# Kernel tuning notes

Measured on AMD Instinct MI355X. Metric: run time of the kernel, lower is better.

## Reference

```python
import jax, jax.numpy as jnp
import numpy as np

D = 1024; H = 16; DKV = 64; DFF = 4096
NB = 32; MAXD = 128
B = 4; LD = 1024; LE = 1024
NEG = -1e9
EPS = 1e-6


def setup_inputs():
    key = jax.random.key(0)
    ks = jax.random.split(key, 13)
    s = 0.02
    def W(k, shape):
        return jax.random.normal(k, shape, jnp.float32) * s
    return {
        "encoder_hidden_states": jax.random.normal(ks[0], (B, LE, D), jnp.float32),
        "hidden_states": jax.random.normal(ks[1], (B, LD, D), jnp.float32),
        "ln1_w": jnp.ones((D,), jnp.float32),
        "sa_q": W(ks[2], (D, H * DKV)),
        "sa_k": W(ks[3], (D, H * DKV)),
        "sa_v": W(ks[4], (D, H * DKV)),
        "sa_o": W(ks[5], (H * DKV, D)),
        "rel_bias": W(ks[6], (NB, H)),
        "ln2_w": jnp.ones((D,), jnp.float32),
        "ca_q": W(ks[7], (D, H * DKV)),
        "ca_k": W(ks[8], (D, H * DKV)),
        "ca_v": W(ks[9], (D, H * DKV)),
        "ca_o": W(ks[10], (H * DKV, D)),
        "ln3_w": jnp.ones((D,), jnp.float32),
        "wi": W(ks[11], (D, DFF)),
        "wo": W(ks[12], (DFF, D)),
        "final_ln_w": jnp.ones((D,), jnp.float32),
        "encoder_attention_mask": jnp.ones((B, LE), jnp.int32),
        "attention_mask": jnp.ones((B, LD), jnp.int32),
    }


def _rms(x, w):
    # T5 LayerNorm: RMS norm, no mean subtraction, no bias
    var = jnp.mean(x * x, axis=-1, keepdims=True)
    return x * jax.lax.rsqrt(var + EPS) * w


def _rel_bucket(rp):
    # T5 relative position bucketing, non-bidirectional (decoder causal)
    n = -jnp.minimum(rp, 0)
    max_exact = NB // 2
    is_small = n < max_exact
    nf = jnp.maximum(n, 1).astype(jnp.float32)
    val_large = max_exact + (
        jnp.log(nf / max_exact) / np.log(MAXD / max_exact) * (NB - max_exact)
    ).astype(jnp.int32)
    val_large = jnp.minimum(val_large, NB - 1)
    return jnp.where(is_small, n, val_large)


def _attn(xq, xkv, Wq, Wk, Wv, Wo, bias):
    b, lq, _ = xq.shape
    lk = xkv.shape[1]
    q = (xq @ Wq).reshape(b, lq, H, DKV)
    k = (xkv @ Wk).reshape(b, lk, H, DKV)
    v = (xkv @ Wv).reshape(b, lk, H, DKV)
    # T5: no 1/sqrt(d) scaling; additive position bias + mask before softmax
    scores = jnp.einsum('bqhd,bkhd->bhqk', q, k) + bias
    p = jax.nn.softmax(scores, axis=-1)
    o = jnp.einsum('bhqk,bkhd->bqhd', p, v).reshape(b, lq, H * DKV)
    return o @ Wo


def reference(encoder_hidden_states, hidden_states, ln1_w, sa_q, sa_k, sa_v, sa_o,
              rel_bias, ln2_w, ca_q, ca_k, ca_v, ca_o, ln3_w, wi, wo, final_ln_w,
              encoder_attention_mask, attention_mask):
    b, ld, _ = hidden_states.shape
    q_pos = jnp.arange(ld)[:, None]
    k_pos = jnp.arange(ld)[None, :]
    pos_bias = rel_bias[_rel_bucket(k_pos - q_pos)].transpose(2, 0, 1)[None]  # [1,H,LD,LD]
    # decoder extended mask: causal AND padding
    self_ok = (k_pos <= q_pos)[None, None] & (attention_mask[:, None, None, :] > 0)
    self_bias = pos_bias + jnp.where(self_ok, 0.0, NEG)
    # cross-attention: encoder padding mask; enc-dec position bias is zeros
    cross_bias = jnp.where(encoder_attention_mask[:, None, None, :] > 0, 0.0, NEG)

    h = hidden_states
    x = _rms(h, ln1_w)
    h = h + _attn(x, x, sa_q, sa_k, sa_v, sa_o, self_bias)
    x = _rms(h, ln2_w)
    h = h + _attn(x, encoder_hidden_states, ca_q, ca_k, ca_v, ca_o, cross_bias)
    x = _rms(h, ln3_w)
    h = h + jax.nn.relu(x @ wi) @ wo
    return _rms(h, final_ln_w)
```

## Files before the change

### kernel.cpp

```cpp
#include <hip/hip_runtime.h>


#define BB   4
#define LDEC 1024
#define LENC 1024
#define DIM  1024
#define NH   16
#define DK   64
#define DFFN 4096
#define NEGF (-1e9f)

typedef unsigned short u16;
typedef __attribute__((ext_vector_type(8))) unsigned short u16x8;
typedef __attribute__((ext_vector_type(8))) short s16x8;
typedef __attribute__((ext_vector_type(4))) float f32x4;

__device__ __forceinline__ float bf2f(u16 u) {
    union { unsigned int i; float f; } c; c.i = ((unsigned int)u) << 16; return c.f;
}
__device__ __forceinline__ u16 f2bf(float f) {
    union { float f; unsigned int i; } c; c.f = f;
    unsigned int x = c.i;
    return (u16)((x + 0x7fffu + ((x >> 16) & 1u)) >> 16);
}
__device__ __forceinline__ bool probe_f32(const void* probe) {
    return ((const u16*)probe)[0] != 0x3F80;
}
__device__ __forceinline__ float ldx(const void* p, long i, bool f32) {
    return f32 ? ((const float*)p)[i] : bf2f(((const u16*)p)[i]);
}
__device__ __forceinline__ float4 ldx4(const void* p, long i, bool f32) {
    if (f32) return ((const float4*)p)[i >> 2];
    ushort4 u = ((const ushort4*)p)[i >> 2];
    return make_float4(bf2f(u.x), bf2f(u.y), bf2f(u.z), bf2f(u.w));
}
__device__ __forceinline__ void stx(void* p, long i, float v, bool f32) {
    if (f32) ((float*)p)[i] = v;
    else     ((u16*)p)[i] = f2bf(v);
}

__device__ __forceinline__ void gload16(const void* g, void* l) {
    __builtin_amdgcn_global_load_lds(
        (const __attribute__((address_space(1))) void*)g,
        (__attribute__((address_space(3))) void*)l, 16, 0, 0);
}

__global__ __launch_bounds__(256) void copy_k(const void* __restrict__ src,
                                              void* __restrict__ dst,
                                              const void* __restrict__ probe, int n) {
    bool pf = probe_f32(probe);
    long bytes = (long)n * (pf ? 4 : 2);
    long off = ((long)blockIdx.x * 256 + threadIdx.x) * 16;
    if (off < bytes)
        *(int4*)((char*)dst + off) = *(const int4*)((const char*)src + off);
}

__global__ __launch_bounds__(256) void cvt_k(const void* __restrict__ src,
                                             u16* __restrict__ dst,
                                             const void* __restrict__ probe, int n4) {
    bool pf = probe_f32(probe);
    int i = blockIdx.x * 256 + threadIdx.x;
    if (i >= n4) return;
    if (pf) {
        float4 f = ((const float4*)src)[i];
        ushort4 o;
        o.x = f2bf(f.x); o.y = f2bf(f.y); o.z = f2bf(f.z); o.w = f2bf(f.w);
        ((ushort4*)dst)[i] = o;
    } else {
        ((ushort4*)dst)[i] = ((const ushort4*)src)[i];
    }
}

struct TPack {
    const void* s[10]; void* d[10];
    int K[10], N[10], t0[11];
};
__global__ __launch_bounds__(256) void transp_k(TPack p, const void* __restrict__ probe) {
    bool pf = probe_f32(probe);
    __shared__ u16 tl[32][33];
    int bid = blockIdx.x;
    int w = 0;
    while (bid >= p.t0[w + 1]) ++w;
    int lt = bid - p.t0[w];
    const int K = p.K[w], N = p.N[w];
    const int ntx = N >> 5;
    const int bn = (lt % ntx) * 32, bk = (lt / ntx) * 32;
    const int c = threadIdx.x & 31, rr = threadIdx.x >> 5;
    const void* s = p.s[w];
    u16* d = (u16*)p.d[w];
#pragma unroll
    for (int i = 0; i < 4; ++i) {
        int r = rr + i * 8;
        long gi = (long)(bk + r) * N + bn + c;
        tl[c][r] = pf ? f2bf(((const float*)s)[gi]) : ((const u16*)s)[gi];
    }
    __syncthreads();
#pragma unroll
    for (int i = 0; i < 4; ++i) {
        int r = rr + i * 8;
        d[(long)(bn + r) * K + bk + c] = tl[r][c];
    }
}

template <int XM, int YM, int CP, int AD>
__global__ __launch_bounds__(256) void rms_k(const void* __restrict__ X,
                                             const void* __restrict__ w,
                                             void* __restrict__ Y,
                                             void* __restrict__ R,
                                             const u16* __restrict__ G,
                                             const void* __restrict__ probe,
                                             long xoff, long yoff) {
    bool pf = probe_f32(probe);
    bool xf = XM && pf, yf = YM && pf;
    const int row = blockIdx.x, t = threadIdx.x;
    const long idx = (long)row * DIM + t * 4;
    float4 xv = ldx4(X, xoff + idx, xf);
    if (AD) {
        float4 gv = ldx4(G, idx, false);
        xv.x += gv.x; xv.y += gv.y; xv.z += gv.z; xv.w += gv.w;
    }
    float ss = xv.x * xv.x;
    ss = fmaf(xv.y, xv.y, ss);
    ss = fmaf(xv.z, xv.z, ss);
    ss = fmaf(xv.w, xv.w, ss);
#pragma unroll
    for (int off = 32; off; off >>= 1) ss += __shfl_xor(ss, off, 64);
    __shared__ float part[4];
    if ((t & 63) == 0) part[t >> 6] = ss;
    __syncthreads();
    float tot = part[0] + part[1] + part[2] + part[3];
    float scale = rsqrtf(tot * (1.f / (float)DIM) + 1e-6f);
    float4 wv = ldx4(w, t * 4, pf);
    if (CP) {
        stx(R, idx + 0, xv.x, pf);
        stx(R, idx + 1, xv.y, pf);
        stx(R, idx + 2, xv.z, pf);
        stx(R, idx + 3, xv.w, pf);
    }
    stx(Y, yoff + idx + 0, xv.x * scale * wv.x, yf);
    stx(Y, yoff + idx + 1, xv.y * scale * wv.y, yf);
    stx(Y, yoff + idx + 2, xv.z * scale * wv.z, yf);
    stx(Y, yoff + idx + 3, xv.w * scale * wv.w, yf);
}

struct Gemm2Arg {
    const u16* A; const u16* BT; void* C;
    long aoff; long boff; long coff; int ldb;
};

template <int EPI, int BM>
__global__ __launch_bounds__(512) void mgemm2_k(Gemm2Arg g0, Gemm2Arg g1, Gemm2Arg g2,
                                                const void* __restrict__ probe,
                                                int M, int N, int K) {
    const bool pf = probe_f32(probe);
    Gemm2Arg ga = (blockIdx.z == 0) ? g0 : (blockIdx.z == 1 ? g1 : g2);
    constexpr int AG = BM / 64;
    constexpr int AFR = BM / 32;

    __shared__ u16 Asm[2][BM * 64];
    __shared__ u16 Bsm[2][128 * 64];

    const int tid = threadIdx.x;
    const int nx = gridDim.x;
    const int nwg = nx * gridDim.y;
    const int L = blockIdx.x + nx * blockIdx.y;
    const int tile = (L & 7) * (nwg >> 3) + (L >> 3);
    const int m_base = (tile / nx) * BM, n_base = (tile % nx) * 128;

    const int w = tid >> 6, lane = tid & 63;
    const int wm = w >> 2, wn = w & 3;
    const int l15 = lane & 15, quad = lane >> 4;
    const int arow8 = lane >> 3;
    const int acg = (lane & 7) ^ arow8;

    const int iters = K >> 6;
    const u16* Ab = ga.A + ga.aoff;
    const u16* Bb = ga.BT + ga.boff;

#pragma unroll
    for (int g = 0; g < AG; ++g)
        gload16(Ab + (long)(m_base + w * (BM / 8) + g * 8 + arow8) * K + acg * 8,
                &Asm[0][(w * (BM / 8) + g * 8) * 64]);
#pragma unroll
    for (int g = 0; g < 2; ++g)
        gload16(Bb + (long)(n_base + w * 16 + g * 8 + arow8) * ga.ldb + acg * 8,
                &Bsm[0][(w * 16 + g * 8) * 64]);

    f32x4 acc[AFR][2] = {};
    int cur = 0;
    for (int it = 0; it < iters; ++it) {
        __syncthreads();
        if (it + 1 < iters) {
            const int k0 = (it + 1) << 6;
#pragma unroll
            for (int g = 0; g < AG; ++g)
                gload16(Ab + (long)(m_base + w * (BM / 8) + g * 8 + arow8) * K + k0 + acg * 8,
                        &Asm[cur ^ 1][(w * (BM / 8) + g * 8) * 64]);
#pragma unroll
            for (int g = 0; g < 2; ++g)
                gload16(Bb + (long)(n_base + w * 16 + g * 8 + arow8) * ga.ldb + k0 + acg * 8,
                        &Bsm[cur ^ 1][(w * 16 + g * 8) * 64]);
        }
#pragma unroll
        for (int s = 0; s < 2; ++s) {
            s16x8 afr[AFR], bfr[2];
#pragma unroll
            for (int i = 0; i < AFR; ++i) {
                int row = wm * (BM / 2) + i * 16 + l15;
                int chunk = ((s << 2) | quad) ^ (row & 7);
                afr[i] = *(const s16x8*)&Asm[cur][row * 64 + chunk * 8];
            }
#pragma unroll
            for (int j = 0; j < 2; ++j) {
                int nr = wn * 32 + j * 16 + l15;
                int chunk = ((s << 2) | quad) ^ (nr & 7);
                bfr[j] = *(const s16x8*)&Bsm[cur][nr * 64 + chunk * 8];
            }
#pragma unroll
            for (int i = 0; i < AFR; ++i)
#pragma unroll
                for (int j = 0; j < 2; ++j)
                    acc[i][j] = __builtin_amdgcn_mfma_f32_16x16x32_bf16(
                        afr[i], bfr[j], acc[i][j], 0, 0, 0);
        }
        cur ^= 1;
    }

#pragma unroll
    for (int i = 0; i < AFR; ++i) {
#pragma unroll
        for (int j = 0; j < 2; ++j) {
            int n = n_base + wn * 32 + j * 16 + l15;
#pragma unroll
            for (int r4 = 0; r4 < 4; ++r4) {
                int m = m_base + wm * (BM / 2) + i * 16 + quad * 4 + r4;
                float v = acc[i][j][r4];
                if (EPI == 1) v = fmaxf(v, 0.f);
                long cidx = ga.coff + (long)m * N + n;
                if (EPI == 2) {
                    v += ldx(ga.C, cidx, pf);
                    stx(ga.C, cidx, v, pf);
                } else {
                    ((u16*)ga.C)[cidx] = f2bf(v);
                }
            }
        }
    }
}

struct GemmArg {
    const void* A; const void* B; void* C;
    long aoff; long boff; long coff; int asrc; int bsrc; int ldb;
};

__device__ __forceinline__ void load_breg(const GemmArg& ga, bool bf, int k0,
                                          int bk2, int bnb, int n_base, u16* breg) {
    long base0 = (long)(k0 + bk2) * ga.ldb + ga.boff + n_base + bnb;
    long base1 = base0 + ga.ldb;
    if (bf) {
        const float4* Bf = (const float4*)ga.B;
#pragma unroll
        for (int r = 0; r < 2; ++r) {
            long b = (r ? base1 : base0) >> 2;
#pragma unroll
            for (int c = 0; c < 2; ++c) {
                float4 f = Bf[b + c];
                breg[r * 8 + c * 4 + 0] = f2bf(f.x);
                breg[r * 8 + c * 4 + 1] = f2bf(f.y);
                breg[r * 8 + c * 4 + 2] = f2bf(f.z);
                breg[r * 8 + c * 4 + 3] = f2bf(f.w);
            }
        }
    } else {
        u16x8 v0 = *(const u16x8*)((const u16*)ga.B + base0);
        u16x8 v1 = *(const u16x8*)((const u16*)ga.B + base1);
#pragma unroll
        for (int i = 0; i < 8; ++i) { breg[i] = v0[i]; breg[8 + i] = v1[i]; }
    }
}

template <int EPI>
__global__ __launch_bounds__(512) void mgemm_k(GemmArg g0, GemmArg g1, GemmArg g2,
                                               const void* __restrict__ probe,
                                               int M, int N, int K) {
    const bool pf = probe_f32(probe);
    GemmArg ga = (blockIdx.z == 0) ? g0 : (blockIdx.z == 1 ? g1 : g2);
    const bool af = (ga.asrc >= 1) && pf;
    const bool bf = (ga.bsrc >= 1) && pf;

    __shared__ u16 Asm[2][128 * 64];
    __shared__ u16 Bsm[128 * 64];

    const int tid = threadIdx.x;
    const int nx = gridDim.x;
    const int nwg = nx * gridDim.y;
    const int L = blockIdx.x + nx * blockIdx.y;
    const int tile = (L & 7) * (nwg >> 3) + (L >> 3);
    const int m_base = (tile / nx) * 128, n_base = (tile % nx) * 128;

    const int w = tid >> 6, lane = tid & 63;
    const int wm = w >> 2, wn = w & 3;
    const int l15 = lane & 15, quad = lane >> 4;

    const int bk2 = (tid & 31) * 2;
    const int bnb = (tid >> 5) * 8;
    const int arow8 = lane >> 3;
    const int acg = (lane & 7) ^ arow8;

    const int iters = K >> 6;
    u16 breg[16];
    load_breg(ga, bf, 0, bk2, bnb, n_base, breg);
    if (!af) {
#pragma unroll
        for (int g = 0; g < 2; ++g) {
            const u16* Ag = (const u16*)ga.A + ga.aoff +
                            (long)(m_base + w * 16 + g * 8 + arow8) * K + acg * 8;
            gload16(Ag, &Asm[0][(w * 16 + g * 8) * 64]);
        }
    }

    f32x4 acc[4][2] = {};

    for (int it = 0; it < iters; ++it) {
        const int cur = it & 1;
        __syncthreads();
        if (af) {
            const int row = tid >> 2;
            const float4* Af = (const float4*)ga.A;
            long gb = ga.aoff + (long)(m_base + row) * K + (it << 6);
#pragma unroll
            for (int c = 0; c < 2; ++c) {
                int cg = (tid & 3) * 2 + c;
                float4 fa = Af[(gb + cg * 8) >> 2];
                float4 fb = Af[((gb + cg * 8) >> 2) + 1];
                u16x8 o;
                o[0] = f2bf(fa.x); o[1] = f2bf(fa.y); o[2] = f2bf(fa.z); o[3] = f2bf(fa.w);
                o[4] = f2bf(fb.x); o[5] = f2bf(fb.y); o[6] = f2bf(fb.z); o[7] = f2bf(fb.w);
                *(u16x8*)&Asm[cur][row * 64 + ((cg ^ (row & 7)) << 3)] = o;
            }
        }
#pragma unroll
        for (int i = 0; i < 8; ++i) {
            int n = bnb + i;
            unsigned int pr = (unsigned int)breg[i] | ((unsigned int)breg[8 + i] << 16);
            *(unsigned int*)&Bsm[n * 64 + (((bk2 >> 3) ^ (n & 7)) << 3) + (bk2 & 7)] = pr;
        }
        __syncthreads();
        if (it + 1 < iters) {
            load_breg(ga, bf, (it + 1) << 6, bk2, bnb, n_base, breg);
            if (!af) {
#pragma unroll
                for (int g = 0; g < 2; ++g) {
                    const u16* Ag = (const u16*)ga.A + ga.aoff +
                                    (long)(m_base + w * 16 + g * 8 + arow8) * K +
                                    ((it + 1) << 6) + acg * 8;
                    gload16(Ag, &Asm[cur ^ 1][(w * 16 + g * 8) * 64]);
                }
            }
        }
#pragma unroll
        for (int s = 0; s < 2; ++s) {
            s16x8 afr[4], bfr[2];
#pragma unroll
            for (int i = 0; i < 4; ++i) {
                int row = wm * 64 + i * 16 + l15;
                int chunk = ((s << 2) | quad) ^ (row & 7);
                afr[i] = *(const s16x8*)&Asm[cur][row * 64 + chunk * 8];
            }
#pragma unroll
            for (int j = 0; j < 2; ++j) {
                int nr = wn * 32 + j * 16 + l15;
                int chunk = ((s << 2) | quad) ^ (nr & 7);
                bfr[j] = *(const s16x8*)&Bsm[nr * 64 + chunk * 8];
            }
#pragma unroll
            for (int i = 0; i < 4; ++i)
#pragma unroll
                for (int j = 0; j < 2; ++j)
                    acc[i][j] = __builtin_amdgcn_mfma_f32_16x16x32_bf16(
                        afr[i], bfr[j], acc[i][j], 0, 0, 0);
        }
    }

#pragma unroll
    for (int i = 0; i < 4; ++i) {
#pragma unroll
        for (int j = 0; j < 2; ++j) {
            int n = n_base + wn * 32 + j * 16 + l15;
#pragma unroll
            for (int r4 = 0; r4 < 4; ++r4) {
                int m = m_base + wm * 64 + i * 16 + quad * 4 + r4;
                float v = acc[i][j][r4];
                if (EPI == 1) v = fmaxf(v, 0.f);
                long cidx = ga.coff + (long)m * N + n;
                if (EPI == 2) {
                    v += ldx(ga.C, cidx, pf);
                    stx(ga.C, cidx, v, pf);
                } else {
                    ((u16*)ga.C)[cidx] = f2bf(v);
                }
            }
        }
    }
}

template <int SELF>
__global__ __launch_bounds__(256) void fattn_k(const u16* __restrict__ Q,
                                               const u16* __restrict__ K,
                                               const u16* __restrict__ V,
                                               const void* __restrict__ relb,
                                               const int* __restrict__ mask,
                                               u16* __restrict__ O,
                                               const void* __restrict__ probe,
                                               int LK, int b0, int bufrows) {
    const bool pf = probe_f32(probe);
    __shared__ u16 Ks[64][72];
    __shared__ u16 Vt[64][72];
    __shared__ u16 Ps[64][72];
    __shared__ float bias_lut[SELF ? 1024 : 1];

    const int t = threadIdx.x;
    const int lane = t & 63, w = t >> 6;
    const int l15 = lane & 15, quad = lane >> 4;

    int x, h, z;
    if (gridDim.z == 4) {
        int lid = blockIdx.x + (int)gridDim.x * (blockIdx.y + (int)gridDim.y * blockIdx.z);
        int q = lid >> 8, r = lid & 255, a = r & 3;
        x = (q == 0) ? a : (q == 1) ? 15 - a : (q == 2) ? 4 + a : 11 - a;
        h = (r >> 2) & 15;
        z = r >> 6;
    } else {
        x = blockIdx.x; h = blockIdx.y; z = blockIdx.z;
    }
    const int q0 = x * 64;
    const int batch = b0 + z;
    const long bv = (long)z * bufrows * DIM;
    const int* mrow = mask + batch * LK;

    if (SELF) {
        for (int i = t; i < 1024; i += 256) {
            int bucket;
            if (i < 16) bucket = i;
            else {
                int vv = 16 + (int)(logf((float)i * 0.0625f) * 7.69436394f);
                bucket = vv < 31 ? vv : 31;
            }
            bias_lut[i] = ldx(relb, bucket * NH + h, pf);
        }
    }

    s16x8 qf[2];
    {
        const u16* qp = Q + bv + (long)(q0 + w * 16 + l15) * DIM + h * DK + quad * 8;
        qf[0] = *(const s16x8*)qp;
        qf[1] = *(const s16x8*)(qp + 32);
    }

    float l_reg[4] = {0.f, 0.f, 0.f, 0.f};
    f32x4 Oa[4] = {};

    const int ntiles = SELF ? (q0 >> 6) + 1 : (LK >> 6);
    const int kr = t >> 2, kseg = t & 3;
    const int kr2 = (t & 31) * 2, dnb = (t >> 5) * 8;

    u16x8 kp0, kp1, vp0, vp1;
    {
        long gb = bv + (long)kr * DIM + h * DK + kseg * 16;
        kp0 = *(const u16x8*)(K + gb);
        kp1 = *(const u16x8*)(K + gb + 8);
        long gv = bv + (long)kr2 * DIM + h * DK + dnb;
        vp0 = *(const u16x8*)(V + gv);
        vp1 = *(const u16x8*)(V + gv + DIM);
    }

    for (int kt = 0; kt < ntiles; ++kt) {
        __syncthreads();
        *(u16x8*)&Ks[kr][kseg * 16] = kp0;
        *(u16x8*)&Ks[kr][kseg * 16 + 8] = kp1;
#pragma unroll
        for (int i = 0; i < 8; ++i) {
            unsigned int pr = (unsigned int)vp0[i] | ((unsigned int)vp1[i] << 16);
            *(unsigned int*)&Vt[dnb + i][kr2] = pr;
        }
        __syncthreads();
        if (kt + 1 < ntiles) {
            long gb = bv + (long)((kt + 1) * 64 + kr) * DIM + h * DK + kseg * 16;
            kp0 = *(const u16x8*)(K + gb);
            kp1 = *(const u16x8*)(K + gb + 8);
            long gv = bv + (long)((kt + 1) * 64 + kr2) * DIM + h * DK + dnb;
            vp0 = *(const u16x8*)(V + gv);
            vp1 = *(const u16x8*)(V + gv + DIM);
        }

        f32x4 sc[4] = {};
#pragma unroll
        for (int j = 0; j < 4; ++j)
#pragma unroll
            for (int s = 0; s < 2; ++s) {
                s16x8 bf = *(const s16x8*)&Ks[j * 16 + l15][s * 32 + quad * 8];
                sc[j] = __builtin_amdgcn_mfma_f32_16x16x32_bf16(qf[s], bf, sc[j], 0, 0, 0);
            }

#pragma unroll
        for (int j = 0; j < 4; ++j) {
            int key = kt * 64 + j * 16 + l15;
            float ma = (mrow[key] > 0) ? 0.f : NEGF;
#pragma unroll
            for (int r = 0; r < 4; ++r) {
                float sv = sc[j][r];
                if (SELF) {
                    int q = q0 + w * 16 + quad * 4 + r;
                    int d = q - key;
                    sv += bias_lut[d < 0 ? 0 : d] + ((key <= q) ? ma : NEGF);
                } else {
                    sv += ma;
                }
                float p = __expf(sv);
                Ps[w * 16 + quad * 4 + r][j * 16 + l15] = f2bf(p);
                l_reg[r] += p;
            }
        }
        asm volatile("" ::: "memory");

#pragma unroll
        for (int s = 0; s < 2; ++s) {
            s16x8 pa = *(const s16x8*)&Ps[w * 16 + l15][s * 32 + quad * 8];
#pragma unroll
            for (int j = 0; j < 4; ++j) {
                s16x8 vb = *(const s16x8*)&Vt[j * 16 + l15][s * 32 + quad * 8];
                Oa[j] = __builtin_amdgcn_mfma_f32_16x16x32_bf16(pa, vb, Oa[j], 0, 0, 0);
            }
        }
    }

#pragma unroll
    for (int r = 0; r < 4; ++r) {
        float v = l_reg[r];
        v += __shfl_xor(v, 1, 64);
        v += __shfl_xor(v, 2, 64);
        v += __shfl_xor(v, 4, 64);
        v += __shfl_xor(v, 8, 64);
        l_reg[r] = 1.f / v;
    }
#pragma unroll
    for (int j = 0; j < 4; ++j)
#pragma unroll
        for (int r = 0; r < 4; ++r) {
            int row = w * 16 + quad * 4 + r;
            O[bv + (long)(q0 + row) * DIM + h * DK + j * 16 + l15] =
                f2bf(Oa[j][r] * l_reg[r]);
        }
}

extern "C" void kernel_launch(void* const* d_in, const int* in_sizes, int n_in,
                              void* d_out, int out_size, void* d_ws, size_t ws_size,
                              hipStream_t stream) {
    const void* enc  = d_in[0];
    const void* hs   = d_in[1];
    const void* ln1  = d_in[2];
    const void* sa_q = d_in[3];
    const void* sa_k = d_in[4];
    const void* sa_v = d_in[5];
    const void* sa_o = d_in[6];
    const void* relb = d_in[7];
    const void* ln2  = d_in[8];
    const void* ca_q = d_in[9];
    const void* ca_k = d_in[10];
    const void* ca_v = d_in[11];
    const void* ca_o = d_in[12];
    const void* ln3  = d_in[13];
    const void* wi   = d_in[14];
    const void* wo   = d_in[15];
    const void* fln  = d_in[16];
    const int* enc_mask = (const int*)d_in[17];
    const int* dec_mask = (const int*)d_in[18];
    void* out = d_out;
    const void* probe = ln1;

    char* ws = (char*)d_ws;
    const int M = BB * LDEC;
    dim3 blk(256), blkG(512);
    GemmArg dz = {nullptr, nullptr, nullptr, 0, 0, 0, 0, 0, 0};
    Gemm2Arg dz2 = {nullptr, nullptr, nullptr, 0, 0, 0, 0};

    if (ws_size >= (72ull << 20)) {
        u16* X0 = (u16*)(ws);
        u16* X1 = (u16*)(ws + (8u  << 20));
        u16* X2 = (u16*)(ws + (16u << 20));
        u16* X3 = (u16*)(ws + (24u << 20));
        u16* FF = X1;
        u16* encB = (u16*)(ws + (32u << 20));
        u16* wT[10];
        wT[0] = (u16*)(ws + (40u << 20));
        wT[1] = (u16*)(ws + (42u << 20));
        wT[2] = (u16*)(ws + (44u << 20));
        wT[3] = (u16*)(ws + (46u << 20));
        wT[4] = (u16*)(ws + (48u << 20));
        wT[5] = (u16*)(ws + (50u << 20));
        wT[6] = (u16*)(ws + (52u << 20));
        wT[7] = (u16*)(ws + (54u << 20));
        wT[8] = (u16*)(ws + (56u << 20));
        wT[9] = (u16*)(ws + (64u << 20));

        cvt_k<<<4096, blk, 0, stream>>>(enc, encB, probe, 1048576);
        {
            TPack p;
            const void* s[10] = {sa_q, sa_k, sa_v, sa_o, ca_q, ca_k, ca_v, ca_o, wi, wo};
            const int kk[10] = {DIM, DIM, DIM, DIM, DIM, DIM, DIM, DIM, DIM, DFFN};
            const int nn[10] = {DIM, DIM, DIM, DIM, DIM, DIM, DIM, DIM, DFFN, DIM};
            int acc = 0;
            for (int i = 0; i < 10; ++i) {
                p.s[i] = s[i]; p.d[i] = wT[i]; p.K[i] = kk[i]; p.N[i] = nn[i];
                p.t0[i] = acc; acc += (kk[i] >> 5) * (nn[i] >> 5);
            }
            p.t0[10] = acc;
            transp_k<<<acc, blk, 0, stream>>>(p, probe);
        }

        dim3 gQKV(8, 64, 3);
        dim3 gOP(8, 64, 1);
        dim3 gWI(16, 64, 2);
        dim3 gAttn(LDEC / 64, NH, BB);

        rms_k<1, 0, 1, 0><<<M, blk, 0, stream>>>(hs, ln1, X0, out, nullptr,
                                                 probe, 0, 0);
        {
            Gemm2Arg zq = {X0, wT[0], X1, 0, 0, 0, DIM};
            Gemm2Arg zk = {X0, wT[1], X2, 0, 0, 0, DIM};
            Gemm2Arg zv = {X0, wT[2], X3, 0, 0, 0, DIM};
            mgemm2_k<0, 64><<<gQKV, blkG, 0, stream>>>(zq, zk, zv, probe, M, DIM, DIM);
        }
        fattn_k<1><<<gAttn, blk, 0, stream>>>(X1, X2, X3, relb, dec_mask, X0,
                                              probe, LDEC, 0, LDEC);
        {
            Gemm2Arg zo = {X0, wT[3], X1, 0, 0, 0, DIM};
            mgemm2_k<0, 64><<<gOP, blkG, 0, stream>>>(zo, dz2, dz2, probe, M, DIM, DIM);
        }

        rms_k<1, 0, 1, 1><<<M, blk, 0, stream>>>(out, ln2, X0, out, X1,
                                                 probe, 0, 0);
        {
            Gemm2Arg zq = {X0, wT[4], X1, 0, 0, 0, DIM};
            Gemm2Arg zk = {encB, wT[5], X2, 0, 0, 0, DIM};
            Gemm2Arg zv = {encB, wT[6], X3, 0, 0, 0, DIM};
            mgemm2_k<0, 64><<<gQKV, blkG, 0, stream>>>(zq, zk, zv, probe, M, DIM, DIM);
        }
        fattn_k<0><<<gAttn, blk, 0, stream>>>(X1, X2, X3, relb, enc_mask, X0,
                                              probe, LENC, 0, LENC);
        {
            Gemm2Arg zo = {X0, wT[7], X1, 0, 0, 0, DIM};
            mgemm2_k<0, 64><<<gOP, blkG, 0, stream>>>(zo, dz2, dz2, probe, M, DIM, DIM);
        }

        rms_k<1, 0, 1, 1><<<M, blk, 0, stream>>>(out, ln3, X0, out, X1,
                                                 probe, 0, 0);
        {
            Gemm2Arg z0 = {X0, wT[8], FF, 0, 0, 0, DIM};
            Gemm2Arg z1 = {X0, wT[8], FF, 0, (long)2048 * DIM, 2048, DIM};
            mgemm2_k<1, 64><<<gWI, blkG, 0, stream>>>(z0, z1, dz2, probe, M, DFFN, DIM);
        }
        {
            Gemm2Arg zo = {FF, wT[9], X0, 0, 0, 0, DFFN};
            mgemm2_k<0, 64><<<gOP, blkG, 0, stream>>>(zo, dz2, dz2, probe, M, DIM, DFFN);
        }

        rms_k<1, 1, 0, 1><<<M, blk, 0, stream>>>(out, fln, out, nullptr, X0,
                                                 probe, 0, 0);
    } else if (ws_size >= (32ull << 20)) {
        u16* X0 = (u16*)(ws);
        u16* X1 = (u16*)(ws + (8u << 20));
        u16* X2 = (u16*)(ws + (16u << 20));
        u16* X3 = (u16*)(ws + (24u << 20));
        u16* FF = X2;
        const bool have_encb = ws_size >= (40ull << 20);
        u16* encB = (u16*)(ws + (32u << 20));

        dim3 gQKV(8, 32, 3);
        dim3 gOP(8, 32, 1);
        dim3 gWI(16, 32, 1);
        dim3 gAttn(LDEC / 64, NH, BB);

        copy_k<<<(M * DIM / 4) / 256, blk, 0, stream>>>(hs, out, probe, M * DIM);
        if (have_encb)
            cvt_k<<<4096, blk, 0, stream>>>(enc, encB, probe, M * DIM / 4);

        rms_k<1, 0, 0, 0><<<M, blk, 0, stream>>>(out, ln1, X0, nullptr, nullptr, probe, 0, 0);
        {
            GemmArg zq = {X0, sa_q, X1, 0, 0, 0, 0, 1, DIM};
            GemmArg zk = {X0, sa_k, X2, 0, 0, 0, 0, 1, DIM};
            GemmArg zv = {X0, sa_v, X3, 0, 0, 0, 0, 1, DIM};
            mgemm_k<0><<<gQKV, blkG, 0, stream>>>(zq, zk, zv, probe, M, DIM, DIM);
        }
        fattn_k<1><<<gAttn, blk, 0, stream>>>(X1, X2, X3, relb, dec_mask, X0,
                                              probe, LDEC, 0, LDEC);
        {
            GemmArg zo = {X0, sa_o, out, 0, 0, 0, 0, 1, DIM};
            mgemm_k<2><<<gOP, blkG, 0, stream>>>(zo, dz, dz, probe, M, DIM, DIM);
        }

        rms_k<1, 0, 0, 0><<<M, blk, 0, stream>>>(out, ln2, X0, nullptr, nullptr, probe, 0, 0);
        {
            const void* encA = have_encb ? (const void*)encB : enc;
            int asrc = have_encb ? 0 : 1;
            GemmArg zq = {X0, ca_q, X1, 0, 0, 0, 0, 1, DIM};
            GemmArg zk = {encA, ca_k, X2, 0, 0, 0, asrc, 1, DIM};
            GemmArg zv = {encA, ca_v, X3, 0, 0, 0, asrc, 1, DIM};
            mgemm_k<0><<<gQKV, blkG, 0, stream>>>(zq, zk, zv, probe, M, DIM, DIM);
        }
        fattn_k<0><<<gAttn, blk, 0, stream>>>(X1, X2, X3, relb, enc_mask, X0,
                                              probe, LENC, 0, LENC);
        {
            GemmArg zo = {X0, ca_o, out, 0, 0, 0, 0, 1, DIM};
            mgemm_k<2><<<gOP, blkG, 0, stream>>>(zo, dz, dz, probe, M, DIM, DIM);
        }

        rms_k<1, 0, 0, 0><<<M, blk, 0, stream>>>(out, ln3, X0, nullptr, nullptr, probe, 0, 0);
        for (int d = 0; d < 2; ++d) {
            GemmArg zi = {X0, wi, FF, 0, (long)d * 2048, 0, 0, 1, DFFN};
            mgemm_k<1><<<gWI, blkG, 0, stream>>>(zi, dz, dz, probe, M, 2048, DIM);
            GemmArg zo = {FF, wo, out, 0, (long)d * 2048 * DIM, 0, 0, 1, DIM};
            mgemm_k<2><<<gOP, blkG, 0, stream>>>(zo, dz, dz, probe, M, DIM, 2048);
        }
        rms_k<1, 1, 0, 0><<<M, blk, 0, stream>>>(out, fln, out, nullptr, nullptr, probe, 0, 0);
        return;
    } else {
        u16* X0 = (u16*)(ws);
        u16* X1 = (u16*)(ws + (2u << 20));
        u16* X2 = (u16*)(ws + (4u << 20));
        u16* X3 = (u16*)(ws + (6u << 20));
        u16* XN = (u16*)(ws);
        u16* FF = (u16*)(ws + (4u << 20));
        dim3 gQKV(8, 8, 3);
        dim3 gOP(8, 8, 1);
        dim3 gFFN(8, 16, 1);
        dim3 gAttn(LDEC / 64, NH, 1);

        copy_k<<<(M * DIM / 4) / 256, blk, 0, stream>>>(hs, out, probe, M * DIM);

        for (int b = 0; b < BB; ++b) {
            const long ob = (long)b * LDEC * DIM;
            const long eb = (long)b * LENC * DIM;

            rms_k<1, 0, 0, 0><<<LDEC, blk, 0, stream>>>(out, ln1, X0, nullptr, nullptr, probe, ob, 0);
            {
                GemmArg zq = {X0, sa_q, X1, 0, 0, 0, 0, 1, DIM};
                GemmArg zk = {X0, sa_k, X2, 0, 0, 0, 0, 1, DIM};
                GemmArg zv = {X0, sa_v, X3, 0, 0, 0, 0, 1, DIM};
                mgemm_k<0><<<gQKV, blkG, 0, stream>>>(zq, zk, zv, probe, LDEC, DIM, DIM);
            }
            fattn_k<1><<<gAttn, blk, 0, stream>>>(X1, X2, X3, relb, dec_mask, X0,
                                                  probe, LDEC, b, 0);
            {
                GemmArg zo = {X0, sa_o, out, 0, 0, ob, 0, 1, DIM};
                mgemm_k<2><<<gOP, blkG, 0, stream>>>(zo, dz, dz, probe, LDEC, DIM, DIM);
            }

            rms_k<1, 0, 0, 0><<<LDEC, blk, 0, stream>>>(out, ln2, X0, nullptr, nullptr, probe, ob, 0);
            {
                GemmArg zq = {X0, ca_q, X1, 0, 0, 0, 0, 1, DIM};
                GemmArg zk = {enc, ca_k, X2, eb, 0, 0, 1, 1, DIM};
                GemmArg zv = {enc, ca_v, X3, eb, 0, 0, 1, 1, DIM};
                mgemm_k<0><<<gQKV, blkG, 0, stream>>>(zq, zk, zv, probe, LENC, DIM, DIM);
            }
            fattn_k<0><<<gAttn, blk, 0, stream>>>(X1, X2, X3, relb, enc_mask, X0,
                                                  probe, LENC, b, 0);
            {
                GemmArg zo = {X0, ca_o, out, 0, 0, ob, 0, 1, DIM};
                mgemm_k<2><<<gOP, blkG, 0, stream>>>(zo, dz, dz, probe, LDEC, DIM, DIM);
            }
        }

        for (int mc = 0; mc < 2; ++mc) {
            const long r0 = (long)mc * 2048;
            rms_k<1, 0, 0, 0><<<2048, blk, 0, stream>>>(out, ln3, XN, nullptr, nullptr, probe, r0 * DIM, 0);
            for (int d = 0; d < 4; ++d) {
                GemmArg zi = {XN, wi, FF, 0, (long)d * 1024, 0, 0, 1, DFFN};
                mgemm_k<1><<<gFFN, blkG, 0, stream>>>(zi, dz, dz, probe, 2048, 1024, DIM);
                GemmArg zo = {FF, wo, out, 0, (long)d * 1024 * DIM, r0 * DIM, 0, 1, DIM};
                mgemm_k<2><<<gFFN, blkG, 0, stream>>>(zo, dz, dz, probe, 2048, DIM, 1024);
            }
        }
        rms_k<1, 1, 0, 0><<<M, blk, 0, stream>>>(out, fln, out, nullptr, nullptr, probe, 0, 0);
        return;
    }
}
```

Measured before the change: 507.1 us.

## Split-K output projections into two halves and sum partials in RMS norm

The attention output and FFN down projections each run as two K-halves in one launch (grid z=2), writing separate partial buffers. The following RMS-norm kernel adds both partials to the residual. This doubles the block count so more of the GPU is busy, at the cost of extra partial-buffer traffic and bf16 rounding of the partial sums. The attention kernel also raises wave priority around its MFMA blocks so the matrix work gets issued sooner. One partial buffer shares its address with a transposed-weight slot, which is a hazard if those weights are reused across calls.

```diff
diff --git a/kernel.cpp b/kernel.cpp
--- a/kernel.cpp
+++ b/kernel.cpp
@@ -108,6 +108,7 @@
                                              void* __restrict__ Y,
                                              void* __restrict__ R,
                                              const u16* __restrict__ G,
+                                             const u16* __restrict__ G2,
                                              const void* __restrict__ probe,
                                              long xoff, long yoff) {
     bool pf = probe_f32(probe);
@@ -115,8 +116,12 @@
     const int row = blockIdx.x, t = threadIdx.x;
     const long idx = (long)row * DIM + t * 4;
     float4 xv = ldx4(X, xoff + idx, xf);
-    if (AD) {
+    if (AD >= 1) {
         float4 gv = ldx4(G, idx, false);
+        xv.x += gv.x; xv.y += gv.y; xv.z += gv.z; xv.w += gv.w;
+    }
+    if (AD >= 2) {
+        float4 gv = ldx4(G2, idx, false);
         xv.x += gv.x; xv.y += gv.y; xv.z += gv.z; xv.w += gv.w;
     }
     float ss = xv.x * xv.x;
@@ -145,7 +150,7 @@
 
 struct Gemm2Arg {
     const u16* A; const u16* BT; void* C;
-    long aoff; long boff; long coff; int ldb;
+    long aoff; long boff; long coff; int ldb; int klen;
 };
 
 template <int EPI, int BM>
@@ -173,7 +178,7 @@
     const int arow8 = lane >> 3;
     const int acg = (lane & 7) ^ arow8;
 
-    const int iters = K >> 6;
+    const int iters = ga.klen >> 6;
     const u16* Ab = ga.A + ga.aoff;
     const u16* Bb = ga.BT + ga.boff;
 
@@ -494,6 +499,7 @@
         }
 
         f32x4 sc[4] = {};
+        __builtin_amdgcn_s_setprio(1);
 #pragma unroll
         for (int j = 0; j < 4; ++j)
 #pragma unroll
@@ -501,6 +507,7 @@
                 s16x8 bf = *(const s16x8*)&Ks[j * 16 + l15][s * 32 + quad * 8];
                 sc[j] = __builtin_amdgcn_mfma_f32_16x16x32_bf16(qf[s], bf, sc[j], 0, 0, 0);
             }
+        __builtin_amdgcn_s_setprio(0);
 
 #pragma unroll
         for (int j = 0; j < 4; ++j) {
@@ -523,6 +530,7 @@
         }
         asm volatile("" ::: "memory");
 
+        __builtin_amdgcn_s_setprio(1);
 #pragma unroll
         for (int s = 0; s < 2; ++s) {
             s16x8 pa = *(const s16x8*)&Ps[w * 16 + l15][s * 32 + quad * 8];
@@ -532,6 +540,7 @@
                 Oa[j] = __builtin_amdgcn_mfma_f32_16x16x32_bf16(pa, vb, Oa[j], 0, 0, 0);
             }
         }
+        __builtin_amdgcn_s_setprio(0);
     }
 
 #pragma unroll
@@ -582,7 +591,7 @@
     const int M = BB * LDEC;
     dim3 blk(256), blkG(512);
     GemmArg dz = {nullptr, nullptr, nullptr, 0, 0, 0, 0, 0, 0};
-    Gemm2Arg dz2 = {nullptr, nullptr, nullptr, 0, 0, 0, 0};
+    Gemm2Arg dz2 = {nullptr, nullptr, nullptr, 0, 0, 0, 0, 0};
 
     if (ws_size >= (72ull << 20)) {
         u16* X0 = (u16*)(ws);
@@ -591,6 +600,7 @@
         u16* X3 = (u16*)(ws + (24u << 20));
         u16* FF = X1;
         u16* encB = (u16*)(ws + (32u << 20));
+        u16* G3b = (u16*)(ws + (40u << 20));
         u16* wT[10];
         wT[0] = (u16*)(ws + (40u << 20));
         wT[1] = (u16*)(ws + (42u << 20));
@@ -619,53 +629,56 @@
         }
 
         dim3 gQKV(8, 64, 3);
-        dim3 gOP(8, 64, 1);
+        dim3 gOP2(8, 64, 2);
         dim3 gWI(16, 64, 2);
         dim3 gAttn(LDEC / 64, NH, BB);
 
-        rms_k<1, 0, 1, 0><<<M, blk, 0, stream>>>(hs, ln1, X0, out, nullptr,
+        rms_k<1, 0, 1, 0><<<M, blk, 0, stream>>>(hs, ln1, X0, out, nullptr, nullptr,
                                                  probe, 0, 0);
         {
-            Gemm2Arg zq = {X0, wT[0], X1, 0, 0, 0, DIM};
-            Gemm2Arg zk = {X0, wT[1], X2, 0, 0, 0, DIM};
-            Gemm2Arg zv = {X0, wT[2], X3, 0, 0, 0, DIM};
+            Gemm2Arg zq = {X0, wT[0], X1, 0, 0, 0, DIM, DIM};
+            Gemm2Arg zk = {X0, wT[1], X2, 0, 0, 0, DIM, DIM};
+            Gemm2Arg zv = {X0, wT[2], X3, 0, 0, 0, DIM, DIM};
             mgemm2_k<0, 64><<<gQKV, blkG, 0, stream>>>(zq, zk, zv, probe, M, DIM, DIM);
         }
         fattn_k<1><<<gAttn, blk, 0, stream>>>(X1, X2, X3, relb, dec_mask, X0,
                                               probe, LDEC, 0, LDEC);
         {
-            Gemm2Arg zo = {X0, wT[3], X1, 0, 0, 0, DIM};
-            mgemm2_k<0, 64><<<gOP, blkG, 0, stream>>>(zo, dz2, dz2, probe, M, DIM, DIM);
-        }
-
-        rms_k<1, 0, 1, 1><<<M, blk, 0, stream>>>(out, ln2, X0, out, X1,
+            Gemm2Arg za = {X0, wT[3], X1, 0, 0, 0, DIM, 512};
+            Gemm2Arg zb = {X0, wT[3], X2, 512, 512, 0, DIM, 512};
+            mgemm2_k<0, 64><<<gOP2, blkG, 0, stream>>>(za, zb, dz2, probe, M, DIM, DIM);
+        }
+
+        rms_k<1, 0, 1, 2><<<M, blk, 0, stream>>>(out, ln2, X0, out, X1, X2,
                                                  probe, 0, 0);
         {
-            Gemm2Arg zq = {X0, wT[4], X1, 0, 0, 0, DIM};
-            Gemm2Arg zk = {encB, wT[5], X2, 0, 0, 0, DIM};
-            Gemm2Arg zv = {encB, wT[6], X3, 0, 0, 0, DIM};
+            Gemm2Arg zq = {X0, wT[4], X1, 0, 0, 0, DIM, DIM};
+            Gemm2Arg zk = {encB, wT[5], X2, 0, 0, 0, DIM, DIM};
+            Gemm2Arg zv = {encB, wT[6], X3, 0, 0, 0, DIM, DIM};
             mgemm2_k<0, 64><<<gQKV, blkG, 0, stream>>>(zq, zk, zv, probe, M, DIM, DIM);
         }
         fattn_k<0><<<gAttn, blk, 0, stream>>>(X1, X2, X3, relb, enc_mask, X0,
                                               probe, LENC, 0, LENC);
         {
-            Gemm2Arg zo = {X0, wT[7], X1, 0, 0, 0, DIM};
-            mgemm2_k<0, 64><<<gOP, blkG, 0, stream>>>(zo, dz2, dz2, probe, M, DIM, DIM);
-        }
-
-        rms_k<1, 0, 1, 1><<<M, blk, 0, stream>>>(out, ln3, X0, out, X1,
+            Gemm2Arg za = {X0, wT[7], X1, 0, 0, 0, DIM, 512};
+            Gemm2Arg zb = {X0, wT[7], X2, 512, 512, 0, DIM, 512};
+            mgemm2_k<0, 64><<<gOP2, blkG, 0, stream>>>(za, zb, dz2, probe, M, DIM, DIM);
+        }
+
+        rms_k<1, 0, 1, 2><<<M, blk, 0, stream>>>(out, ln3, X0, out, X1, X2,
                                                  probe, 0, 0);
         {
-            Gemm2Arg z0 = {X0, wT[8], FF, 0, 0, 0, DIM};
-            Gemm2Arg z1 = {X0, wT[8], FF, 0, (long)2048 * DIM, 2048, DIM};
+            Gemm2Arg z0 = {X0, wT[8], FF, 0, 0, 0, DIM, DIM};
+            Gemm2Arg z1 = {X0, wT[8], FF, 0, (long)2048 * DIM, 2048, DIM, DIM};
             mgemm2_k<1, 64><<<gWI, blkG, 0, stream>>>(z0, z1, dz2, probe, M, DFFN, DIM);
         }
         {
-            Gemm2Arg zo = {FF, wT[9], X0, 0, 0, 0, DFFN};
-            mgemm2_k<0, 64><<<gOP, blkG, 0, stream>>>(zo, dz2, dz2, probe, M, DIM, DFFN);
-        }
-
-        rms_k<1, 1, 0, 1><<<M, blk, 0, stream>>>(out, fln, out, nullptr, X0,
+            Gemm2Arg za = {FF, wT[9], X0, 0, 0, 0, DFFN, 2048};
+            Gemm2Arg zb = {FF, wT[9], G3b, 2048, 2048, 0, DFFN, 2048};
+            mgemm2_k<0, 64><<<gOP2, blkG, 0, stream>>>(za, zb, dz2, probe, M, DIM, DFFN);
+        }
+
+        rms_k<1, 1, 0, 2><<<M, blk, 0, stream>>>(out, fln, out, nullptr, X0, G3b,
                                                  probe, 0, 0);
     } else if (ws_size >= (32ull << 20)) {
         u16* X0 = (u16*)(ws);
@@ -685,7 +698,7 @@
         if (have_encb)
             cvt_k<<<4096, blk, 0, stream>>>(enc, encB, probe, M * DIM / 4);
 
-        rms_k<1, 0, 0, 0><<<M, blk, 0, stream>>>(out, ln1, X0, nullptr, nullptr, probe, 0, 0);
+        rms_k<1, 0, 0, 0><<<M, blk, 0, stream>>>(out, ln1, X0, nullptr, nullptr, nullptr, probe, 0, 0);
         {
             GemmArg zq = {X0, sa_q, X1, 0, 0, 0, 0, 1, DIM};
             GemmArg zk = {X0, sa_k, X2, 0, 0, 0, 0, 1, DIM};
@@ -699,7 +712,7 @@
             mgemm_k<2><<<gOP, blkG, 0, stream>>>(zo, dz, dz, probe, M, DIM, DIM);
         }
 
-        rms_k<1, 0, 0, 0><<<M, blk, 0, stream>>>(out, ln2, X0, nullptr, nullptr, probe, 0, 0);
+        rms_k<1, 0, 0, 0><<<M, blk, 0, stream>>>(out, ln2, X0, nullptr, nullptr, nullptr, probe, 0, 0);
         {
             const void* encA = have_encb ? (const void*)encB : enc;
             int asrc = have_encb ? 0 : 1;
@@ -715,14 +728,14 @@
             mgemm_k<2><<<gOP, blkG, 0, stream>>>(zo, dz, dz, probe, M, DIM, DIM);
         }
 
-        rms_k<1, 0, 0, 0><<<M, blk, 0, stream>>>(out, ln3, X0, nullptr, nullptr, probe, 0, 0);
+        rms_k<1, 0, 0, 0><<<M, blk, 0, stream>>>(out, ln3, X0, nullptr, nullptr, nullptr, probe, 0, 0);
         for (int d = 0; d < 2; ++d) {
             GemmArg zi = {X0, wi, FF, 0, (long)d * 2048, 0, 0, 1, DFFN};
             mgemm_k<1><<<gWI, blkG, 0, stream>>>(zi, dz, dz, probe, M, 2048, DIM);
             GemmArg zo = {FF, wo, out, 0, (long)d * 2048 * DIM, 0, 0, 1, DIM};
             mgemm_k<2><<<gOP, blkG, 0, stream>>>(zo, dz, dz, probe, M, DIM, 2048);
         }
-        rms_k<1, 1, 0, 0><<<M, blk, 0, stream>>>(out, fln, out, nullptr, nullptr, probe, 0, 0);
+        rms_k<1, 1, 0, 0><<<M, blk, 0, stream>>>(out, fln, out, nullptr, nullptr, nullptr, probe, 0, 0);
         return;
     } else {
         u16* X0 = (u16*)(ws);
@@ -742,7 +755,7 @@
             const long ob = (long)b * LDEC * DIM;
             const long eb = (long)b * LENC * DIM;
 
-            rms_k<1, 0, 0, 0><<<LDEC, blk, 0, stream>>>(out, ln1, X0, nullptr, nullptr, probe, ob, 0);
+            rms_k<1, 0, 0, 0><<<LDEC, blk, 0, stream>>>(out, ln1, X0, nullptr, nullptr, nullptr, probe, ob, 0);
             {
                 GemmArg zq = {X0, sa_q, X1, 0, 0, 0, 0, 1, DIM};
                 GemmArg zk = {X0, sa_k, X2, 0, 0, 0, 0, 1, DIM};
@@ -756,7 +769,7 @@
                 mgemm_k<2><<<gOP, blkG, 0, stream>>>(zo, dz, dz, probe, LDEC, DIM, DIM);
             }
 
-            rms_k<1, 0, 0, 0><<<LDEC, blk, 0, stream>>>(out, ln2, X0, nullptr, nullptr, probe, ob, 0);
+            rms_k<1, 0, 0, 0><<<LDEC, blk, 0, stream>>>(out, ln2, X0, nullptr, nullptr, nullptr, probe, ob, 0);
             {
                 GemmArg zq = {X0, ca_q, X1, 0, 0, 0, 0, 1, DIM};
                 GemmArg zk = {enc, ca_k, X2, eb, 0, 0, 1, 1, DIM};
@@ -773,7 +786,7 @@
 
         for (int mc = 0; mc < 2; ++mc) {
             const long r0 = (long)mc * 2048;
-            rms_k<1, 0, 0, 0><<<2048, blk, 0, stream>>>(out, ln3, XN, nullptr, nullptr, probe, r0 * DIM, 0);
+            rms_k<1, 0, 0, 0><<<2048, blk, 0, stream>>>(out, ln3, XN, nullptr, nullptr, nullptr, probe, r0 * DIM, 0);
             for (int d = 0; d < 4; ++d) {
                 GemmArg zi = {XN, wi, FF, 0, (long)d * 1024, 0, 0, 1, DFFN};
                 mgemm_k<1><<<gFFN, blkG, 0, stream>>>(zi, dz, dz, probe, 2048, 1024, DIM);
@@ -781,7 +794,7 @@
                 mgemm_k<2><<<gFFN, blkG, 0, stream>>>(zo, dz, dz, probe, 2048, DIM, 1024);
             }
         }
-        rms_k<1, 1, 0, 0><<<M, blk, 0, stream>>>(out, fln, out, nullptr, nullptr, probe, 0, 0);
+        rms_k<1, 1, 0, 0><<<M, blk, 0, stream>>>(out, fln, out, nullptr, nullptr, nullptr, probe, 0, 0);
         return;
     }
 }
```

New measurement: 500.8 us. No clear change (-1.2%).
